# Optimization experiments

Hardware: AMD Instinct MI355X
Metric: run time of the kernel (lower is better)

The kernel has to match this reference:

```python
import jax, jax.numpy as jnp
import numpy as np

B, N, D, HEADS, P, C = 64, 197, 768, 12, 12, 200
ARC_S, ARC_M = 30.0, 0.5


def layer_norm(x, g, b, eps=1e-5):
    m = jnp.mean(x, axis=-1, keepdims=True)
    v = jnp.var(x, axis=-1, keepdims=True)
    return (x - m) / jnp.sqrt(v + eps) * g + b


def setup_inputs() -> dict:
    key = jax.random.key(0)
    ks = jax.random.split(key, 16)
    sc = 0.02
    return {
        'hidden': jax.random.normal(ks[0], (B, N, D), jnp.float32),
        'attns': jax.random.uniform(ks[1], (4, B, HEADS, N, N), jnp.float32),
        'labels': jax.random.randint(ks[2], (B,), 0, C),
        'ln1_g': jnp.ones((D,), jnp.float32),
        'ln1_b': jnp.zeros((D,), jnp.float32),
        'w_in': jax.random.normal(ks[3], (3 * D, D), jnp.float32) * sc,
        'b_in': jnp.zeros((3 * D,), jnp.float32),
        'w_out': jax.random.normal(ks[4], (D, D), jnp.float32) * sc,
        'b_out': jnp.zeros((D,), jnp.float32),
        'ln2_g': jnp.ones((D,), jnp.float32),
        'ln2_b': jnp.zeros((D,), jnp.float32),
        'w_pool': jax.random.normal(ks[5], (1, D), jnp.float32) * sc,
        'b_pool': jnp.zeros((1,), jnp.float32),
        'pool_temp': jnp.float32(1.0),
        'w_mlp': jax.random.normal(ks[6], (D, D), jnp.float32) * sc,
        'b_mlp': jnp.zeros((D,), jnp.float32),
        'arc_w': jax.random.normal(ks[7], (C, 2 * D), jnp.float32) * sc,
    }


def reference(hidden, attns, labels, ln1_g, ln1_b, w_in, b_in, w_out, b_out,
              ln2_g, ln2_b, w_pool, b_pool, pool_temp, w_mlp, b_mlp, arc_w):
    cls_embed = hidden[:, 0]              # [B, D]
    patch_embeds = hidden[:, 1:]          # [B, N-1, D]

    # Multi-layer attention fusion: mean over heads, CLS row, drop CLS col.
    attn_scores = attns.mean(axis=2)[:, :, 0, 1:].mean(axis=0)  # [B, N-1]

    # Top-k part selection + gather.
    idx = jax.lax.top_k(attn_scores, P)[1]                       # [B, P]
    parts = jnp.take_along_axis(patch_embeds, idx[:, :, None], axis=1)  # [B,P,D]
    parts = layer_norm(parts, ln1_g, ln1_b)

    # Multi-head self-attention over parts (eval mode, no dropout).
    hd = D // HEADS
    qkv = parts @ w_in.T + b_in                                  # [B,P,3D]
    q, k, v = jnp.split(qkv, 3, axis=-1)
    def heads(t):
        return t.reshape(B, P, HEADS, hd).transpose(0, 2, 1, 3)  # [B,H,P,hd]
    q, k, v = heads(q), heads(k), heads(v)
    scores = jnp.einsum('bhqd,bhkd->bhqk', q, k) / jnp.sqrt(jnp.float32(hd))
    a = jax.nn.softmax(scores, axis=-1)
    o = jnp.einsum('bhqk,bhkd->bhqd', a, v)
    o = o.transpose(0, 2, 1, 3).reshape(B, P, D)
    attn_out = o @ w_out.T + b_out
    attn_out = layer_norm(attn_out, ln2_g, ln2_b)

    # Temperature-softmax weighted pooling.
    raw_w = (attn_out @ w_pool.T + b_pool)[..., 0]               # [B,P]
    weights = jax.nn.softmax(raw_w / jnp.maximum(pool_temp, 0.3), axis=1)
    part_feat = jnp.sum(attn_out * weights[..., None], axis=1)   # [B,D]
    part_feat = jax.nn.relu(part_feat @ w_mlp.T + b_mlp)

    fusion = jnp.concatenate([cls_embed, part_feat], axis=1)     # [B,2D]

    # ArcFace margin (train logits with labels).
    fn = fusion / jnp.linalg.norm(fusion, axis=-1, keepdims=True)
    wn = arc_w / jnp.linalg.norm(arc_w, axis=-1, keepdims=True)
    cosine = fn @ wn.T                                           # [B,C]
    sine = jnp.sqrt(jnp.clip(1.0 - cosine ** 2, 0.0, 1.0))
    cos_m, sin_m = np.cos(ARC_M), np.sin(ARC_M)
    th = np.cos(np.pi - ARC_M)
    mm = np.sin(np.pi - ARC_M) * ARC_M
    phi = cosine * cos_m - sine * sin_m
    phi = jnp.where(cosine > th, phi, cosine - mm)
    one_hot = jax.nn.one_hot(labels, C, dtype=cosine.dtype)
    logits = (one_hot * phi + (1.0 - one_hot) * cosine) * ARC_S
    return logits
```

## Files before the change

### kernel.cpp

```cpp
#include <hip/hip_runtime.h>
#include <hip/hip_bf16.h>
#include <float.h>
#include <math.h>

#define BB 64
#define NNtok 197
#define DD 768
#define HH 12
#define PP 12
#define CC 200
#define NPATCH 196

typedef short bf16x8 __attribute__((ext_vector_type(8)));
typedef float f32x4 __attribute__((ext_vector_type(4)));

__device__ __forceinline__ unsigned short bf16_bits(float x) {
  __hip_bfloat16 h = __float2bfloat16(x);
  return *reinterpret_cast<unsigned short*>(&h);
}
__device__ __forceinline__ float u2f(unsigned int u) {
  union { unsigned int u; float f; } cv; cv.u = u; return cv.f;
}
__device__ __forceinline__ float bfu(unsigned short us) {
  union { unsigned int u; float f; } cv; cv.u = ((unsigned int)us) << 16; return cv.f;
}

__global__ __launch_bounds__(256) void k1_front(
    const float* __restrict__ hidden, const float* __restrict__ attns,
    const float* __restrict__ g, const float* __restrict__ be,
    const float* __restrict__ w1, const float* __restrict__ w2,
    const float* __restrict__ w3, __hip_bfloat16* __restrict__ o1,
    __hip_bfloat16* __restrict__ o2, __hip_bfloat16* __restrict__ o3,
    __hip_bfloat16* __restrict__ parts) {
  int t = threadIdx.x, bi = blockIdx.x;
  if (bi >= 64) {
    for (int i = (bi - 64) * 256 + t; i < 737280; i += 256 * 256) {
      const float* src; __hip_bfloat16* dst; int off;
      if (i < 442368) { src = w1; dst = o1; off = i; }
      else if (i < 589824) { src = w2; dst = o2; off = i - 442368; }
      else { src = w3; dst = o3; off = i - 589824; }
      float4 v = ((const float4*)src)[off];
      union { unsigned short u[4]; ushort4 v4; } p;
      p.u[0] = bf16_bits(v.x); p.u[1] = bf16_bits(v.y);
      p.u[2] = bf16_bits(v.z); p.u[3] = bf16_bits(v.w);
      ((ushort4*)dst)[off] = p.v4;
    }
    return;
  }
  int b = bi;
  __shared__ float sc[256];
  __shared__ int sel_s[PP];
  int wv = t >> 6, ln = t & 63;
  float acc = -FLT_MAX;
  if (t < NPATCH) {
    acc = 0.f;
#pragma unroll
    for (int l = 0; l < 4; l++) {
      float part = 0.f;
#pragma unroll
      for (int h = 0; h < HH; h++) {
        size_t base = (size_t)((l * BB + b) * HH + h) * ((size_t)NNtok * NNtok);
        part += attns[base + 1 + t];
      }
      acc += part * (1.f / 12.f);
    }
    acc *= 0.25f;
  }
  sc[t] = acc;
  __syncthreads();
  if (t < 64) {
    float v[4]; int idx[4];
#pragma unroll
    for (int j = 0; j < 4; j++) { idx[j] = t + j * 64; v[j] = sc[idx[j]]; }
    for (int it = 0; it < PP; ++it) {
      float bv = v[0]; int bidx = idx[0];
#pragma unroll
      for (int j = 1; j < 4; j++)
        if (v[j] > bv || (v[j] == bv && idx[j] < bidx)) { bv = v[j]; bidx = idx[j]; }
      float cv = bv; int ci = bidx;
#pragma unroll
      for (int off = 32; off > 0; off >>= 1) {
        float ov = __shfl_xor(cv, off); int oi = __shfl_xor(ci, off);
        if (ov > cv || (ov == cv && oi < ci)) { cv = ov; ci = oi; }
      }
      if (t == 0) sel_s[it] = ci;
#pragma unroll
      for (int j = 0; j < 4; j++)
        if (idx[j] == ci) v[j] = -FLT_MAX;
    }
  }
  __syncthreads();
#pragma unroll
  for (int q = 0; q < 3; q++) {
    int i = wv * 3 + q;
    const float* row = hidden + ((size_t)b * NNtok + 1 + sel_s[i]) * DD;
    float x[12], s1 = 0.f, s2 = 0.f;
#pragma unroll
    for (int k = 0; k < 12; k++) {
      x[k] = row[ln + 64 * k];
      s1 += x[k]; s2 += x[k] * x[k];
    }
#pragma unroll
    for (int off = 32; off > 0; off >>= 1) {
      s1 += __shfl_xor(s1, off); s2 += __shfl_xor(s2, off);
    }
    float m = s1 * (1.f / DD);
    float rstd = rsqrtf(s2 * (1.f / DD) - m * m + 1e-5f);
    __hip_bfloat16* outp_ = parts + ((size_t)b * PP + i) * DD;
#pragma unroll
    for (int k = 0; k < 12; k++) {
      int d = ln + 64 * k;
      outp_[d] = __float2bfloat16((x[k] - m) * rstd * g[d] + be[d]);
    }
  }
}

__global__ __launch_bounds__(256) void k2_mid(
    const __hip_bfloat16* __restrict__ parts, const __hip_bfloat16* __restrict__ w_in_bf,
    const float* __restrict__ b_in, const __hip_bfloat16* __restrict__ w_out_bf,
    float* __restrict__ part_ws) {
  int bi = blockIdx.x;
  int b = bi >> 2, hg = bi & 3;
  int t = threadIdx.x;
  int wave = t >> 6, lane = t & 63, lr = lane & 15, kg = lane >> 4;
  __shared__ __align__(16) unsigned short qkv3[3][16][192];
  __shared__ __align__(16) unsigned short o3[16][192];
  __shared__ float scores[432];

  int pr = lr < 12 ? lr : 11;
  const __hip_bfloat16* Ab = parts + ((size_t)b * 12 + pr) * DD + kg * 8;
  int wrow[9];
#pragma unroll
  for (int nf = 0; nf < 9; nf++) {
    int lc = wave * 144 + nf * 16 + lr;
    int s = lc / 192, d2 = lc - s * 192;
    wrow[nf] = s * 768 + hg * 192 + d2;
  }
  f32x4 acc[9];
#pragma unroll
  for (int nf = 0; nf < 9; nf++) { acc[nf][0]=0.f; acc[nf][1]=0.f; acc[nf][2]=0.f; acc[nf][3]=0.f; }
  for (int k0 = 0; k0 < 768; k0 += 32) {
    bf16x8 af = *(const bf16x8*)(Ab + k0);
    bf16x8 wf[9];
#pragma unroll
    for (int nf = 0; nf < 9; nf++)
      wf[nf] = *(const bf16x8*)(w_in_bf + (size_t)wrow[nf] * DD + kg * 8 + k0);
#pragma unroll
    for (int nf = 0; nf < 9; nf++)
      acc[nf] = __builtin_amdgcn_mfma_f32_16x16x32_bf16(af, wf[nf], acc[nf], 0, 0, 0);
  }
#pragma unroll
  for (int nf = 0; nf < 9; nf++) {
    int lc = wave * 144 + nf * 16 + lr;
    int s = lc / 192, d2 = lc - s * 192;
    float bv = b_in[s * 768 + hg * 192 + d2];
#pragma unroll
    for (int r = 0; r < 4; r++) {
      int p = kg * 4 + r;
      qkv3[s][p][d2] = bf16_bits(acc[nf][r] + bv);
    }
  }
  __syncthreads();

  for (int e = t; e < 432; e += 256) {
    int h = e / 144, rem = e - h * 144;
    int i = rem / 12, j = rem - i * 12;
    float s = 0.f;
#pragma unroll
    for (int d = 0; d < 64; d++)
      s += bfu(qkv3[0][i][h * 64 + d]) * bfu(qkv3[1][j][h * 64 + d]);
    scores[e] = s * 0.125f;
  }
  __syncthreads();
  if (t < 36) {
    int h = t / 12, i = t - h * 12;
    float* row = scores + h * 144 + i * 12;
    float m = -FLT_MAX;
#pragma unroll
    for (int j = 0; j < 12; j++) m = fmaxf(m, row[j]);
    float e2[12], sum = 0.f;
#pragma unroll
    for (int j = 0; j < 12; j++) { e2[j] = expf(row[j] - m); sum += e2[j]; }
    float inv = 1.f / sum;
#pragma unroll
    for (int j = 0; j < 12; j++) row[j] = e2[j] * inv;
  }
  __syncthreads();
  for (int o = t; o < 2304; o += 256) {
    int i = o / 192, d2 = o - i * 192;
    int h = d2 >> 6;
    float s = 0.f;
#pragma unroll
    for (int j = 0; j < 12; j++)
      s += scores[h * 144 + i * 12 + j] * bfu(qkv3[2][j][d2]);
    o3[i][d2] = bf16_bits(s);
  }
  __syncthreads();

  f32x4 acc2[12];
#pragma unroll
  for (int jf = 0; jf < 12; jf++) { acc2[jf][0]=0.f; acc2[jf][1]=0.f; acc2[jf][2]=0.f; acc2[jf][3]=0.f; }
  const unsigned short* Ob = &o3[0][0] + lr * 192 + kg * 8;
  for (int k0 = 0; k0 < 192; k0 += 32) {
    bf16x8 af = *(const bf16x8*)(Ob + k0);
    bf16x8 wf[12];
#pragma unroll
    for (int jf = 0; jf < 12; jf++) {
      int j = wave * 192 + jf * 16 + lr;
      wf[jf] = *(const bf16x8*)(w_out_bf + (size_t)j * DD + hg * 192 + kg * 8 + k0);
    }
#pragma unroll
    for (int jf = 0; jf < 12; jf++)
      acc2[jf] = __builtin_amdgcn_mfma_f32_16x16x32_bf16(af, wf[jf], acc2[jf], 0, 0, 0);
  }
#pragma unroll
  for (int jf = 0; jf < 12; jf++) {
    int j = wave * 192 + jf * 16 + lr;
#pragma unroll
    for (int r = 0; r < 4; r++) {
      int p = kg * 4 + r;
      if (p < 12)
        part_ws[(((size_t)b * 4 + hg) * 12 + p) * DD + j] = acc2[jf][r];
    }
  }
}

__global__ __launch_bounds__(256) void k3_back(
    const float* __restrict__ part_ws, const float* __restrict__ b_out,
    const float* __restrict__ g, const float* __restrict__ be,
    const float* __restrict__ wp, const float* __restrict__ bp,
    const float* __restrict__ ptemp, const __hip_bfloat16* __restrict__ wmlp,
    const float* __restrict__ bmlp, float* __restrict__ pmlp) {
  int bi = blockIdx.x;
  int b = bi >> 2, q4 = bi & 3;
  int t = threadIdx.x, wv = t >> 6, ln = t & 63;
  __shared__ float a12[12 * 768];
  __shared__ float raww_s[12];
  __shared__ float pfeat[768];
  for (int u = t; u < 9216; u += 256) {
    int j = u % 768;
    float s = b_out[j];
#pragma unroll
    for (int hg = 0; hg < 4; hg++)
      s += part_ws[(((size_t)b * 4 + hg) * 12) * DD + u];
    a12[u] = s;
  }
  __syncthreads();
#pragma unroll
  for (int q = 0; q < 3; q++) {
    int r = wv * 3 + q;
    float x[12], s1 = 0.f, s2 = 0.f;
#pragma unroll
    for (int k = 0; k < 12; k++) {
      x[k] = a12[r * 768 + ln + 64 * k];
      s1 += x[k]; s2 += x[k] * x[k];
    }
#pragma unroll
    for (int off = 32; off > 0; off >>= 1) {
      s1 += __shfl_xor(s1, off); s2 += __shfl_xor(s2, off);
    }
    float m = s1 * (1.f / DD);
    float rstd = rsqrtf(s2 * (1.f / DD) - m * m + 1e-5f);
    float pl = 0.f;
#pragma unroll
    for (int k = 0; k < 12; k++) {
      int d = ln + 64 * k;
      float y = (x[k] - m) * rstd * g[d] + be[d];
      a12[r * 768 + d] = y;
      pl += y * wp[d];
    }
#pragma unroll
    for (int off = 32; off > 0; off >>= 1) pl += __shfl_xor(pl, off);
    if (ln == 0) raww_s[r] = pl + bp[0];
  }
  __syncthreads();
  float wts[12];
  {
    float inv = 1.f / fmaxf(ptemp[0], 0.3f);
    float z[12], mx = -FLT_MAX;
#pragma unroll
    for (int p = 0; p < 12; p++) { z[p] = raww_s[p] * inv; mx = fmaxf(mx, z[p]); }
    float s = 0.f;
#pragma unroll
    for (int p = 0; p < 12; p++) { z[p] = expf(z[p] - mx); s += z[p]; }
    float is = 1.f / s;
#pragma unroll
    for (int p = 0; p < 12; p++) wts[p] = z[p] * is;
  }
  for (int d = t; d < 768; d += 256) {
    float s = 0.f;
#pragma unroll
    for (int p = 0; p < 12; p++) s += a12[p * 768 + d] * wts[p];
    pfeat[d] = s;
  }
  __syncthreads();
  if (t < 192) {
    int j = q4 * 192 + t;
    const uint4* wr = (const uint4*)(wmlp + (size_t)j * DD);
    float acc2 = bmlp[j];
    for (int k = 0; k < 96; k++) {
      uint4 w4 = wr[k];
      const float* pf = &pfeat[k * 8];
      acc2 += pf[0] * u2f(w4.x << 16) + pf[1] * u2f(w4.x & 0xFFFF0000u)
            + pf[2] * u2f(w4.y << 16) + pf[3] * u2f(w4.y & 0xFFFF0000u)
            + pf[4] * u2f(w4.z << 16) + pf[5] * u2f(w4.z & 0xFFFF0000u)
            + pf[6] * u2f(w4.w << 16) + pf[7] * u2f(w4.w & 0xFFFF0000u);
    }
    pmlp[(size_t)b * DD + j] = fmaxf(acc2, 0.f);
  }
}

__global__ __launch_bounds__(256) void k4_arc(
    const float* __restrict__ hidden, const float* __restrict__ pmlp,
    const float* __restrict__ aw, const int* __restrict__ labels,
    float* __restrict__ out) {
  int cb = blockIdx.x, b = blockIdx.y, t = threadIdx.x;
  int wv = t >> 6, ln = t & 63;
  __shared__ float4 fs4[384];
  __shared__ float a4[4];
  const float4* cls4 = (const float4*)(hidden + (size_t)b * NNtok * DD);
  const float4* pm4 = (const float4*)(pmlp + (size_t)b * DD);
  for (int u = t; u < 384; u += 256) fs4[u] = (u < 192) ? cls4[u] : pm4[u - 192];
  __syncthreads();
  float s = 0.f;
  for (int u = t; u < 384; u += 256) {
    float4 v = fs4[u];
    s += v.x * v.x + v.y * v.y + v.z * v.z + v.w * v.w;
  }
#pragma unroll
  for (int off = 32; off > 0; off >>= 1) s += __shfl_xor(s, off);
  if (ln == 0) a4[wv] = s;
  __syncthreads();
  float rnf = rsqrtf(a4[0] + a4[1] + a4[2] + a4[3]);
  int lab = labels[b];
  const float cos_m = 0.8775825618903728f, sin_m = 0.479425538604203f;
  const float th = -0.8775825618903728f, mm = 0.2397127693021015f;
#pragma unroll
  for (int ci = 0; ci < 4; ci++) {
    int c = cb * 16 + ci * 4 + wv;
    if (c < CC) {
      const float4* wr = (const float4*)(aw + (size_t)c * 1536);
      float acc = 0.f, nw = 0.f;
#pragma unroll
      for (int k = 0; k < 6; k++) {
        float4 a = fs4[ln + 64 * k];
        float4 w = wr[ln + 64 * k];
        acc += a.x * w.x + a.y * w.y + a.z * w.z + a.w * w.w;
        nw += w.x * w.x + w.y * w.y + w.z * w.z + w.w * w.w;
      }
#pragma unroll
      for (int off = 32; off > 0; off >>= 1) {
        acc += __shfl_xor(acc, off); nw += __shfl_xor(nw, off);
      }
      if (ln == 0) {
        float cosv = acc * rsqrtf(nw) * rnf;
        float s2 = 1.f - cosv * cosv;
        s2 = fminf(fmaxf(s2, 0.f), 1.f);
        float sinv = sqrtf(s2);
        float phi = cosv * cos_m - sinv * sin_m;
        phi = (cosv > th) ? phi : (cosv - mm);
        out[(size_t)b * CC + c] = ((c == lab) ? phi : cosv) * 30.f;
      }
    }
  }
}

extern "C" void kernel_launch(void* const* d_in, const int* in_sizes, int n_in,
                              void* d_out, int out_size, void* d_ws, size_t ws_size,
                              hipStream_t stream) {
  const float* hidden = (const float*)d_in[0];
  const float* attns  = (const float*)d_in[1];
  const int*   labels = (const int*)d_in[2];
  const float* ln1_g  = (const float*)d_in[3];
  const float* ln1_b  = (const float*)d_in[4];
  const float* w_in   = (const float*)d_in[5];
  const float* b_in   = (const float*)d_in[6];
  const float* w_out  = (const float*)d_in[7];
  const float* b_out  = (const float*)d_in[8];
  const float* ln2_g  = (const float*)d_in[9];
  const float* ln2_b  = (const float*)d_in[10];
  const float* w_pool = (const float*)d_in[11];
  const float* b_pool = (const float*)d_in[12];
  const float* ptemp  = (const float*)d_in[13];
  const float* w_mlp  = (const float*)d_in[14];
  const float* b_mlp  = (const float*)d_in[15];
  const float* arc_w  = (const float*)d_in[16];
  float* outp = (float*)d_out;

  float* F = (float*)d_ws;
  float* part_ws = F;
  float* pmlp    = F + 2359296;
  __hip_bfloat16* parts_bf = (__hip_bfloat16*)(F + 2408448);
  __hip_bfloat16* w_in_bf  = (__hip_bfloat16*)(F + 2703360);
  __hip_bfloat16* w_out_bf = (__hip_bfloat16*)(F + 3588096);
  __hip_bfloat16* w_mlp_bf = (__hip_bfloat16*)(F + 3883008);

  k1_front<<<320, 256, 0, stream>>>(hidden, attns, ln1_g, ln1_b, w_in, w_out,
                                    w_mlp, w_in_bf, w_out_bf, w_mlp_bf, parts_bf);
  k2_mid<<<256, 256, 0, stream>>>(parts_bf, w_in_bf, b_in, w_out_bf, part_ws);
  k3_back<<<256, 256, 0, stream>>>(part_ws, b_out, ln2_g, ln2_b, w_pool, b_pool,
                                   ptemp, w_mlp_bf, b_mlp, pmlp);
  k4_arc<<<dim3(13, BB), 256, 0, stream>>>(hidden, pmlp, arc_w, labels, outp);
}
```

Measured before the change: 90.79 us.

## Fuse front and mid kernels, convert weights to bf16 on the fly, two batches per block

Merges attention-score top-k selection, LayerNorm gather and the QKV/attention/out-projection work into one kernel. Parts stay in shared memory instead of passing through global memory. Weights are now read as fp32 and converted to bf16 in registers, which removes the separate weight-conversion pass and its extra write and read traffic. Each block handles two batch rows so every weight fragment feeds two MFMAs. The costs are twice the fp32 weight bytes loaded per fragment, fewer blocks (128 with large shared memory), and the MLP in the back kernel now reads fp32 weights.

```diff
diff --git a/kernel.cpp b/kernel.cpp
--- a/kernel.cpp
+++ b/kernel.cpp
@@ -18,218 +18,246 @@
   __hip_bfloat16 h = __float2bfloat16(x);
   return *reinterpret_cast<unsigned short*>(&h);
 }
-__device__ __forceinline__ float u2f(unsigned int u) {
-  union { unsigned int u; float f; } cv; cv.u = u; return cv.f;
-}
 __device__ __forceinline__ float bfu(unsigned short us) {
   union { unsigned int u; float f; } cv; cv.u = ((unsigned int)us) << 16; return cv.f;
 }
-
-__global__ __launch_bounds__(256) void k1_front(
+__device__ __forceinline__ bf16x8 cvt8(float4 a, float4 b) {
+  union { unsigned short u[8]; bf16x8 v; } r;
+  r.u[0] = bf16_bits(a.x); r.u[1] = bf16_bits(a.y);
+  r.u[2] = bf16_bits(a.z); r.u[3] = bf16_bits(a.w);
+  r.u[4] = bf16_bits(b.x); r.u[5] = bf16_bits(b.y);
+  r.u[6] = bf16_bits(b.z); r.u[7] = bf16_bits(b.w);
+  return r.v;
+}
+
+#define OS_PARTS 0
+#define OS_O3 0
+#define OS_SCORES 12288
+#define OS_SC 14016
+#define OS_QKV 37248
+#define OS_SEL 74112
+#define SMB_A 74208
+
+__global__ __launch_bounds__(256, 1) void kA_mid(
     const float* __restrict__ hidden, const float* __restrict__ attns,
-    const float* __restrict__ g, const float* __restrict__ be,
-    const float* __restrict__ w1, const float* __restrict__ w2,
-    const float* __restrict__ w3, __hip_bfloat16* __restrict__ o1,
-    __hip_bfloat16* __restrict__ o2, __hip_bfloat16* __restrict__ o3,
-    __hip_bfloat16* __restrict__ parts) {
-  int t = threadIdx.x, bi = blockIdx.x;
-  if (bi >= 64) {
-    for (int i = (bi - 64) * 256 + t; i < 737280; i += 256 * 256) {
-      const float* src; __hip_bfloat16* dst; int off;
-      if (i < 442368) { src = w1; dst = o1; off = i; }
-      else if (i < 589824) { src = w2; dst = o2; off = i - 442368; }
-      else { src = w3; dst = o3; off = i - 589824; }
-      float4 v = ((const float4*)src)[off];
-      union { unsigned short u[4]; ushort4 v4; } p;
-      p.u[0] = bf16_bits(v.x); p.u[1] = bf16_bits(v.y);
-      p.u[2] = bf16_bits(v.z); p.u[3] = bf16_bits(v.w);
-      ((ushort4*)dst)[off] = p.v4;
-    }
-    return;
-  }
-  int b = bi;
-  __shared__ float sc[256];
-  __shared__ int sel_s[PP];
+    const float* __restrict__ ln1_g, const float* __restrict__ ln1_b,
+    const float* __restrict__ w_in, const float* __restrict__ b_in,
+    const float* __restrict__ w_out, float* __restrict__ part_ws) {
+  __shared__ __align__(16) char sm[SMB_A];
+  int t = threadIdx.x, blk = blockIdx.x;
   int wv = t >> 6, ln = t & 63;
-  float acc = -FLT_MAX;
-  if (t < NPATCH) {
-    acc = 0.f;
-#pragma unroll
-    for (int l = 0; l < 4; l++) {
-      float part = 0.f;
-#pragma unroll
-      for (int h = 0; h < HH; h++) {
-        size_t base = (size_t)((l * BB + b) * HH + h) * ((size_t)NNtok * NNtok);
-        part += attns[base + 1 + t];
-      }
-      acc += part * (1.f / 12.f);
-    }
-    acc *= 0.25f;
-  }
-  sc[t] = acc;
-  __syncthreads();
-  if (t < 64) {
-    float v[4]; int idx[4];
-#pragma unroll
-    for (int j = 0; j < 4; j++) { idx[j] = t + j * 64; v[j] = sc[idx[j]]; }
-    for (int it = 0; it < PP; ++it) {
-      float bv = v[0]; int bidx = idx[0];
-#pragma unroll
-      for (int j = 1; j < 4; j++)
-        if (v[j] > bv || (v[j] == bv && idx[j] < bidx)) { bv = v[j]; bidx = idx[j]; }
-      float cv = bv; int ci = bidx;
-#pragma unroll
-      for (int off = 32; off > 0; off >>= 1) {
-        float ov = __shfl_xor(cv, off); int oi = __shfl_xor(ci, off);
-        if (ov > cv || (ov == cv && oi < ci)) { cv = ov; ci = oi; }
-      }
-      if (t == 0) sel_s[it] = ci;
-#pragma unroll
-      for (int j = 0; j < 4; j++)
-        if (idx[j] == ci) v[j] = -FLT_MAX;
-    }
-  }
-  __syncthreads();
+  int hg = blk & 3, bp = blk >> 2;
+  int b0 = bp * 2;
+  unsigned short* partsL = (unsigned short*)(sm + OS_PARTS);
+  unsigned short* qkvp = (unsigned short*)(sm + OS_QKV);
+  unsigned short* o3p = (unsigned short*)(sm + OS_O3);
+  float* scores = (float*)(sm + OS_SCORES);
+  float* sc = (float*)(sm + OS_SC);
+  int* sel_s = (int*)(sm + OS_SEL);
+
+#pragma unroll
+  for (int bq = 0; bq < 2; bq++) {
+    int b = b0 + bq;
+    float acc = -FLT_MAX;
+    if (t < NPATCH) {
+      acc = 0.f;
+#pragma unroll
+      for (int l = 0; l < 4; l++) {
+        float part = 0.f;
+#pragma unroll
+        for (int h = 0; h < HH; h++) {
+          size_t base = (size_t)((l * BB + b) * HH + h) * ((size_t)NNtok * NNtok);
+          part += attns[base + 1 + t];
+        }
+        acc += part * (1.f / 12.f);
+      }
+      acc *= 0.25f;
+    }
+    sc[t] = acc;
+    __syncthreads();
+    if (t < 64) {
+      float v[4]; int idx[4];
+#pragma unroll
+      for (int j = 0; j < 4; j++) { idx[j] = t + j * 64; v[j] = sc[idx[j]]; }
+      for (int it = 0; it < PP; ++it) {
+        float bv = v[0]; int bidx = idx[0];
+#pragma unroll
+        for (int j = 1; j < 4; j++)
+          if (v[j] > bv || (v[j] == bv && idx[j] < bidx)) { bv = v[j]; bidx = idx[j]; }
+        float cv = bv; int ci = bidx;
+#pragma unroll
+        for (int off = 32; off > 0; off >>= 1) {
+          float ov = __shfl_xor(cv, off); int oi = __shfl_xor(ci, off);
+          if (ov > cv || (ov == cv && oi < ci)) { cv = ov; ci = oi; }
+        }
+        if (t == 0) sel_s[bq * 12 + it] = ci;
+#pragma unroll
+        for (int j = 0; j < 4; j++)
+          if (idx[j] == ci) v[j] = -FLT_MAX;
+      }
+    }
+    __syncthreads();
+  }
+
 #pragma unroll
   for (int q = 0; q < 3; q++) {
     int i = wv * 3 + q;
-    const float* row = hidden + ((size_t)b * NNtok + 1 + sel_s[i]) * DD;
-    float x[12], s1 = 0.f, s2 = 0.f;
-#pragma unroll
-    for (int k = 0; k < 12; k++) {
-      x[k] = row[ln + 64 * k];
-      s1 += x[k]; s2 += x[k] * x[k];
-    }
-#pragma unroll
-    for (int off = 32; off > 0; off >>= 1) {
-      s1 += __shfl_xor(s1, off); s2 += __shfl_xor(s2, off);
-    }
-    float m = s1 * (1.f / DD);
-    float rstd = rsqrtf(s2 * (1.f / DD) - m * m + 1e-5f);
-    __hip_bfloat16* outp_ = parts + ((size_t)b * PP + i) * DD;
-#pragma unroll
-    for (int k = 0; k < 12; k++) {
-      int d = ln + 64 * k;
-      outp_[d] = __float2bfloat16((x[k] - m) * rstd * g[d] + be[d]);
-    }
-  }
-}
-
-__global__ __launch_bounds__(256) void k2_mid(
-    const __hip_bfloat16* __restrict__ parts, const __hip_bfloat16* __restrict__ w_in_bf,
-    const float* __restrict__ b_in, const __hip_bfloat16* __restrict__ w_out_bf,
-    float* __restrict__ part_ws) {
-  int bi = blockIdx.x;
-  int b = bi >> 2, hg = bi & 3;
-  int t = threadIdx.x;
-  int wave = t >> 6, lane = t & 63, lr = lane & 15, kg = lane >> 4;
-  __shared__ __align__(16) unsigned short qkv3[3][16][192];
-  __shared__ __align__(16) unsigned short o3[16][192];
-  __shared__ float scores[432];
-
-  int pr = lr < 12 ? lr : 11;
-  const __hip_bfloat16* Ab = parts + ((size_t)b * 12 + pr) * DD + kg * 8;
-  int wrow[9];
-#pragma unroll
-  for (int nf = 0; nf < 9; nf++) {
-    int lc = wave * 144 + nf * 16 + lr;
-    int s = lc / 192, d2 = lc - s * 192;
-    wrow[nf] = s * 768 + hg * 192 + d2;
-  }
-  f32x4 acc[9];
-#pragma unroll
-  for (int nf = 0; nf < 9; nf++) { acc[nf][0]=0.f; acc[nf][1]=0.f; acc[nf][2]=0.f; acc[nf][3]=0.f; }
-  for (int k0 = 0; k0 < 768; k0 += 32) {
-    bf16x8 af = *(const bf16x8*)(Ab + k0);
-    bf16x8 wf[9];
-#pragma unroll
-    for (int nf = 0; nf < 9; nf++)
-      wf[nf] = *(const bf16x8*)(w_in_bf + (size_t)wrow[nf] * DD + kg * 8 + k0);
-#pragma unroll
-    for (int nf = 0; nf < 9; nf++)
-      acc[nf] = __builtin_amdgcn_mfma_f32_16x16x32_bf16(af, wf[nf], acc[nf], 0, 0, 0);
-  }
-#pragma unroll
-  for (int nf = 0; nf < 9; nf++) {
-    int lc = wave * 144 + nf * 16 + lr;
-    int s = lc / 192, d2 = lc - s * 192;
-    float bv = b_in[s * 768 + hg * 192 + d2];
-#pragma unroll
-    for (int r = 0; r < 4; r++) {
-      int p = kg * 4 + r;
-      qkv3[s][p][d2] = bf16_bits(acc[nf][r] + bv);
-    }
-  }
-  __syncthreads();
-
-  for (int e = t; e < 432; e += 256) {
-    int h = e / 144, rem = e - h * 144;
-    int i = rem / 12, j = rem - i * 12;
-    float s = 0.f;
-#pragma unroll
-    for (int d = 0; d < 64; d++)
-      s += bfu(qkv3[0][i][h * 64 + d]) * bfu(qkv3[1][j][h * 64 + d]);
-    scores[e] = s * 0.125f;
-  }
-  __syncthreads();
-  if (t < 36) {
-    int h = t / 12, i = t - h * 12;
-    float* row = scores + h * 144 + i * 12;
-    float m = -FLT_MAX;
-#pragma unroll
-    for (int j = 0; j < 12; j++) m = fmaxf(m, row[j]);
-    float e2[12], sum = 0.f;
-#pragma unroll
-    for (int j = 0; j < 12; j++) { e2[j] = expf(row[j] - m); sum += e2[j]; }
-    float inv = 1.f / sum;
-#pragma unroll
-    for (int j = 0; j < 12; j++) row[j] = e2[j] * inv;
-  }
-  __syncthreads();
-  for (int o = t; o < 2304; o += 256) {
-    int i = o / 192, d2 = o - i * 192;
-    int h = d2 >> 6;
-    float s = 0.f;
-#pragma unroll
-    for (int j = 0; j < 12; j++)
-      s += scores[h * 144 + i * 12 + j] * bfu(qkv3[2][j][d2]);
-    o3[i][d2] = bf16_bits(s);
-  }
-  __syncthreads();
-
-  f32x4 acc2[12];
-#pragma unroll
-  for (int jf = 0; jf < 12; jf++) { acc2[jf][0]=0.f; acc2[jf][1]=0.f; acc2[jf][2]=0.f; acc2[jf][3]=0.f; }
-  const unsigned short* Ob = &o3[0][0] + lr * 192 + kg * 8;
-  for (int k0 = 0; k0 < 192; k0 += 32) {
-    bf16x8 af = *(const bf16x8*)(Ob + k0);
-    bf16x8 wf[12];
+#pragma unroll
+    for (int bq = 0; bq < 2; bq++) {
+      const float* row =
+          hidden + ((size_t)(b0 + bq) * NNtok + 1 + sel_s[bq * 12 + i]) * DD;
+      float x[12], s1 = 0.f, s2 = 0.f;
+#pragma unroll
+      for (int k = 0; k < 12; k++) {
+        x[k] = row[ln + 64 * k];
+        s1 += x[k]; s2 += x[k] * x[k];
+      }
+#pragma unroll
+      for (int off = 32; off > 0; off >>= 1) {
+        s1 += __shfl_xor(s1, off); s2 += __shfl_xor(s2, off);
+      }
+      float m = s1 * (1.f / DD);
+      float rstd = rsqrtf(s2 * (1.f / DD) - m * m + 1e-5f);
+#pragma unroll
+      for (int k = 0; k < 12; k++) {
+        int d = ln + 64 * k;
+        partsL[(bq * 12 + i) * 776 + d] =
+            bf16_bits((x[k] - m) * rstd * ln1_g[d] + ln1_b[d]);
+      }
+    }
+  }
+  __syncthreads();
+
+  {
+    int lr = ln & 15, kg = ln >> 4;
+    int pr = lr < 12 ? lr : 11;
+    int wrow[9];
+#pragma unroll
+    for (int nf = 0; nf < 9; nf++) {
+      int lc = wv * 144 + nf * 16 + lr;
+      int s = lc / 192, d2 = lc - s * 192;
+      wrow[nf] = s * 768 + hg * 192 + d2;
+    }
+    f32x4 acc[2][9];
+#pragma unroll
+    for (int bq = 0; bq < 2; bq++)
+#pragma unroll
+      for (int nf = 0; nf < 9; nf++) {
+        acc[bq][nf][0] = 0.f; acc[bq][nf][1] = 0.f;
+        acc[bq][nf][2] = 0.f; acc[bq][nf][3] = 0.f;
+      }
+    for (int k0 = 0; k0 < 768; k0 += 32) {
+      bf16x8 af0 = *(const bf16x8*)(partsL + (0 * 12 + pr) * 776 + kg * 8 + k0);
+      bf16x8 af1 = *(const bf16x8*)(partsL + (1 * 12 + pr) * 776 + kg * 8 + k0);
+#pragma unroll
+      for (int nf = 0; nf < 9; nf++) {
+        const float* wp = w_in + (size_t)wrow[nf] * DD + kg * 8 + k0;
+        bf16x8 wf = cvt8(*(const float4*)wp, *(const float4*)(wp + 4));
+        acc[0][nf] = __builtin_amdgcn_mfma_f32_16x16x32_bf16(af0, wf, acc[0][nf], 0, 0, 0);
+        acc[1][nf] = __builtin_amdgcn_mfma_f32_16x16x32_bf16(af1, wf, acc[1][nf], 0, 0, 0);
+      }
+    }
+    __syncthreads();
+#pragma unroll
+    for (int nf = 0; nf < 9; nf++) {
+      int lc = wv * 144 + nf * 16 + lr;
+      int s = lc / 192, d2 = lc - s * 192;
+      float bv = b_in[s * 768 + hg * 192 + d2];
+#pragma unroll
+      for (int r = 0; r < 4; r++) {
+        int p = kg * 4 + r;
+        if (p < 12) {
+          qkvp[(0 * 48 + s * 16 + p) * 192 + d2] = bf16_bits(acc[0][nf][r] + bv);
+          qkvp[(1 * 48 + s * 16 + p) * 192 + d2] = bf16_bits(acc[1][nf][r] + bv);
+        }
+      }
+    }
+  }
+  __syncthreads();
+
+#pragma unroll
+  for (int bq = 0; bq < 2; bq++) {
+    const unsigned short* qk = qkvp + bq * 9216;
+    unsigned short* o3 = o3p + bq * 3072;
+    for (int e = t; e < 432; e += 256) {
+      int h = e / 144, rem = e - h * 144;
+      int i = rem / 12, j = rem - i * 12;
+      float s = 0.f;
+#pragma unroll
+      for (int d = 0; d < 64; d++)
+        s += bfu(qk[(0 * 16 + i) * 192 + h * 64 + d]) *
+             bfu(qk[(1 * 16 + j) * 192 + h * 64 + d]);
+      scores[e] = s * 0.125f;
+    }
+    __syncthreads();
+    if (t < 36) {
+      int h = t / 12, i = t - h * 12;
+      float* row = scores + h * 144 + i * 12;
+      float m = -FLT_MAX;
+#pragma unroll
+      for (int j = 0; j < 12; j++) m = fmaxf(m, row[j]);
+      float e2[12], sum = 0.f;
+#pragma unroll
+      for (int j = 0; j < 12; j++) { e2[j] = expf(row[j] - m); sum += e2[j]; }
+      float inv = 1.f / sum;
+#pragma unroll
+      for (int j = 0; j < 12; j++) row[j] = e2[j] * inv;
+    }
+    __syncthreads();
+    for (int o = t; o < 2304; o += 256) {
+      int i = o / 192, d2 = o - i * 192;
+      int h = d2 >> 6;
+      float s = 0.f;
+#pragma unroll
+      for (int j = 0; j < 12; j++)
+        s += scores[h * 144 + i * 12 + j] * bfu(qk[(2 * 16 + j) * 192 + d2]);
+      o3[i * 192 + d2] = bf16_bits(s);
+    }
+    __syncthreads();
+  }
+
+  {
+    int lr = ln & 15, kg = ln >> 4;
+    f32x4 acc2[2][12];
+#pragma unroll
+    for (int bq = 0; bq < 2; bq++)
+#pragma unroll
+      for (int jf = 0; jf < 12; jf++) {
+        acc2[bq][jf][0] = 0.f; acc2[bq][jf][1] = 0.f;
+        acc2[bq][jf][2] = 0.f; acc2[bq][jf][3] = 0.f;
+      }
+    for (int k0 = 0; k0 < 192; k0 += 32) {
+      bf16x8 af0 = *(const bf16x8*)(o3p + 0 * 3072 + lr * 192 + kg * 8 + k0);
+      bf16x8 af1 = *(const bf16x8*)(o3p + 1 * 3072 + lr * 192 + kg * 8 + k0);
+#pragma unroll
+      for (int jf = 0; jf < 12; jf++) {
+        int j = wv * 192 + jf * 16 + lr;
+        const float* wp = w_out + (size_t)j * DD + hg * 192 + kg * 8 + k0;
+        bf16x8 wf = cvt8(*(const float4*)wp, *(const float4*)(wp + 4));
+        acc2[0][jf] = __builtin_amdgcn_mfma_f32_16x16x32_bf16(af0, wf, acc2[0][jf], 0, 0, 0);
+        acc2[1][jf] = __builtin_amdgcn_mfma_f32_16x16x32_bf16(af1, wf, acc2[1][jf], 0, 0, 0);
+      }
+    }
 #pragma unroll
     for (int jf = 0; jf < 12; jf++) {
-      int j = wave * 192 + jf * 16 + lr;
-      wf[jf] = *(const bf16x8*)(w_out_bf + (size_t)j * DD + hg * 192 + kg * 8 + k0);
-    }
-#pragma unroll
-    for (int jf = 0; jf < 12; jf++)
-      acc2[jf] = __builtin_amdgcn_mfma_f32_16x16x32_bf16(af, wf[jf], acc2[jf], 0, 0, 0);
-  }
-#pragma unroll
-  for (int jf = 0; jf < 12; jf++) {
-    int j = wave * 192 + jf * 16 + lr;
-#pragma unroll
-    for (int r = 0; r < 4; r++) {
-      int p = kg * 4 + r;
-      if (p < 12)
-        part_ws[(((size_t)b * 4 + hg) * 12 + p) * DD + j] = acc2[jf][r];
-    }
-  }
-}
-
-__global__ __launch_bounds__(256) void k3_back(
+      int j = wv * 192 + jf * 16 + lr;
+#pragma unroll
+      for (int r = 0; r < 4; r++) {
+        int p = kg * 4 + r;
+        if (p < 12) {
+          part_ws[(((size_t)b0 * 4 + hg) * 12 + p) * DD + j] = acc2[0][jf][r];
+          part_ws[(((size_t)(b0 + 1) * 4 + hg) * 12 + p) * DD + j] = acc2[1][jf][r];
+        }
+      }
+    }
+  }
+}
+
+__global__ __launch_bounds__(256) void kB_back(
     const float* __restrict__ part_ws, const float* __restrict__ b_out,
     const float* __restrict__ g, const float* __restrict__ be,
     const float* __restrict__ wp, const float* __restrict__ bp,
-    const float* __restrict__ ptemp, const __hip_bfloat16* __restrict__ wmlp,
+    const float* __restrict__ ptemp, const float* __restrict__ w_mlp,
     const float* __restrict__ bmlp, float* __restrict__ pmlp) {
   int bi = blockIdx.x;
   int b = bi >> 2, q4 = bi & 3;
@@ -296,21 +324,18 @@
   __syncthreads();
   if (t < 192) {
     int j = q4 * 192 + t;
-    const uint4* wr = (const uint4*)(wmlp + (size_t)j * DD);
+    const float4* wr = (const float4*)(w_mlp + (size_t)j * DD);
     float acc2 = bmlp[j];
-    for (int k = 0; k < 96; k++) {
-      uint4 w4 = wr[k];
-      const float* pf = &pfeat[k * 8];
-      acc2 += pf[0] * u2f(w4.x << 16) + pf[1] * u2f(w4.x & 0xFFFF0000u)
-            + pf[2] * u2f(w4.y << 16) + pf[3] * u2f(w4.y & 0xFFFF0000u)
-            + pf[4] * u2f(w4.z << 16) + pf[5] * u2f(w4.z & 0xFFFF0000u)
-            + pf[6] * u2f(w4.w << 16) + pf[7] * u2f(w4.w & 0xFFFF0000u);
+    for (int k = 0; k < 192; k++) {
+      float4 w4 = wr[k];
+      const float* pf = &pfeat[k * 4];
+      acc2 += pf[0] * w4.x + pf[1] * w4.y + pf[2] * w4.z + pf[3] * w4.w;
     }
     pmlp[(size_t)b * DD + j] = fmaxf(acc2, 0.f);
   }
 }
 
-__global__ __launch_bounds__(256) void k4_arc(
+__global__ __launch_bounds__(256) void kC_arc(
     const float* __restrict__ hidden, const float* __restrict__ pmlp,
     const float* __restrict__ aw, const int* __restrict__ labels,
     float* __restrict__ out) {
@@ -389,16 +414,11 @@
 
   float* F = (float*)d_ws;
   float* part_ws = F;
-  float* pmlp    = F + 2359296;
-  __hip_bfloat16* parts_bf = (__hip_bfloat16*)(F + 2408448);
-  __hip_bfloat16* w_in_bf  = (__hip_bfloat16*)(F + 2703360);
-  __hip_bfloat16* w_out_bf = (__hip_bfloat16*)(F + 3588096);
-  __hip_bfloat16* w_mlp_bf = (__hip_bfloat16*)(F + 3883008);
-
-  k1_front<<<320, 256, 0, stream>>>(hidden, attns, ln1_g, ln1_b, w_in, w_out,
-                                    w_mlp, w_in_bf, w_out_bf, w_mlp_bf, parts_bf);
-  k2_mid<<<256, 256, 0, stream>>>(parts_bf, w_in_bf, b_in, w_out_bf, part_ws);
-  k3_back<<<256, 256, 0, stream>>>(part_ws, b_out, ln2_g, ln2_b, w_pool, b_pool,
-                                   ptemp, w_mlp_bf, b_mlp, pmlp);
-  k4_arc<<<dim3(13, BB), 256, 0, stream>>>(hidden, pmlp, arc_w, labels, outp);
-}
+  float* pmlp = F + 2359296;
+
+  kA_mid<<<128, 256, 0, stream>>>(hidden, attns, ln1_g, ln1_b, w_in, b_in,
+                                  w_out, part_ws);
+  kB_back<<<256, 256, 0, stream>>>(part_ws, b_out, ln2_g, ln2_b, w_pool, b_pool,
+                                   ptemp, w_mlp, b_mlp, pmlp);
+  kC_arc<<<dim3(13, BB), 256, 0, stream>>>(hidden, pmlp, arc_w, labels, outp);
+}
```

Result: slower. 181.6 us (+100.1%).
